# Kernel tuning notes

Measured on AMD Instinct MI355X. Metric: run time of the kernel, lower is better.

Reference implementation:

```python
import jax, jax.numpy as jnp
import numpy as np


def setup_inputs() -> dict:
    key = jax.random.key(0)
    B, C, H, W = 16, 96, 128, 128
    x = jax.random.normal(key, (B, C, H, W), dtype=jnp.float32)
    return {"x": x}


def reference(x):
    # CrossScan forward, in_channel_first=True, out_channel_first=True,
    # one_by_one=False, scans=0 (4-directional cross scan).
    B, C, H, W = x.shape
    y0 = x.reshape(B, C, H * W)                       # row-major scan
    y1 = jnp.swapaxes(x, 2, 3).reshape(B, C, H * W)   # column-major scan
    y2 = y0[..., ::-1]                                # reversed row-major
    y3 = y1[..., ::-1]                                # reversed column-major
    return jnp.stack([y0, y1, y2, y3], axis=1)        # [B, 4, C, H*W]
```

## Files before the change

kernel.cpp:

```cpp
#include <hip/hip_runtime.h>


#define Hh 128
#define Ww 128
#define HWp (Hh * Ww)
#define Cc 96
#define Bb 16
#define TILE 64

__global__ __launch_bounds__(1024) void cross_scan_kernel(
    const float* __restrict__ x, float* __restrict__ out) {
  __shared__ float tile[TILE][TILE + 1];

  const int tx = threadIdx.x;
  const int ty = threadIdx.y;
  const int tileId = blockIdx.x;
  const int tileRow = (tileId >> 1) * TILE;
  const int tileCol = (tileId & 1) * TILE;
  const int plane = blockIdx.y;
  const int b = plane / Cc;
  const int c = plane - b * Cc;

  const float* xp = x + (size_t)plane * HWp;
  float* out0 = out + ((size_t)(b * 4 + 0) * Cc + c) * HWp;
  float* out1 = out + ((size_t)(b * 4 + 1) * Cc + c) * HWp;
  float* out2 = out + ((size_t)(b * 4 + 2) * Cc + c) * HWp;
  float* out3 = out + ((size_t)(b * 4 + 3) * Cc + c) * HWp;

  const int row = tileRow + ty;
  const int col = tileCol + tx * 4;
  const int idx = row * Ww + col;

  const float4 v = *(const float4*)(xp + idx);

  *(float4*)(out0 + idx) = v;
  *(float4*)(out2 + (HWp - 4 - idx)) = make_float4(v.w, v.z, v.y, v.x);

  tile[ty][tx * 4 + 0] = v.x;
  tile[ty][tx * 4 + 1] = v.y;
  tile[ty][tx * 4 + 2] = v.z;
  tile[ty][tx * 4 + 3] = v.w;
  __syncthreads();

  float4 t;
  t.x = tile[tx * 4 + 0][ty];
  t.y = tile[tx * 4 + 1][ty];
  t.z = tile[tx * 4 + 2][ty];
  t.w = tile[tx * 4 + 3][ty];
  const int o = (tileCol + ty) * Hh + tileRow + tx * 4;
  *(float4*)(out1 + o) = t;
  *(float4*)(out3 + (HWp - 4 - o)) = make_float4(t.w, t.z, t.y, t.x);
}

extern "C" void kernel_launch(void* const* d_in, const int* in_sizes, int n_in,
                              void* d_out, int out_size, void* d_ws,
                              size_t ws_size, hipStream_t stream) {
  const float* x = (const float*)d_in[0];
  float* out = (float*)d_out;
  dim3 grid(4, Bb * Cc);
  dim3 block(16, 64);
  cross_scan_kernel<<<grid, block, 0, stream>>>(x, out);
}
```

Measured before the change: 463.0 us.

## Use smaller blocks with per-thread row loops and shared-memory reversed outputs

Shrinks blocks from 1024 to 256 threads, with each thread loading and storing four rows of the 64x64 tile. The reversed row-major and column-major outputs are now built by reading the shared tile in reverse order, so all four output streams are written with forward, aligned float4 stores. This aims to improve occupancy and memory-level parallelism on a bandwidth-bound copy. In exchange it adds extra shared-memory reads and possible bank conflicts for the reversed reads.

```diff
diff --git a/kernel.cpp b/kernel.cpp
--- a/kernel.cpp
+++ b/kernel.cpp
@@ -8,15 +8,15 @@
 #define Bb 16
 #define TILE 64
 
-__global__ __launch_bounds__(1024) void cross_scan_kernel(
+__global__ __launch_bounds__(256) void cross_scan_kernel(
     const float* __restrict__ x, float* __restrict__ out) {
   __shared__ float tile[TILE][TILE + 1];
 
   const int tx = threadIdx.x;
   const int ty = threadIdx.y;
   const int tileId = blockIdx.x;
-  const int tileRow = (tileId >> 1) * TILE;
-  const int tileCol = (tileId & 1) * TILE;
+  const int r0 = (tileId >> 1) * TILE;
+  const int c0 = (tileId & 1) * TILE;
   const int plane = blockIdx.y;
   const int b = plane / Cc;
   const int c = plane - b * Cc;
@@ -27,29 +27,54 @@
   float* out2 = out + ((size_t)(b * 4 + 2) * Cc + c) * HWp;
   float* out3 = out + ((size_t)(b * 4 + 3) * Cc + c) * HWp;
 
-  const int row = tileRow + ty;
-  const int col = tileCol + tx * 4;
-  const int idx = row * Ww + col;
-
-  const float4 v = *(const float4*)(xp + idx);
-
-  *(float4*)(out0 + idx) = v;
-  *(float4*)(out2 + (HWp - 4 - idx)) = make_float4(v.w, v.z, v.y, v.x);
-
-  tile[ty][tx * 4 + 0] = v.x;
-  tile[ty][tx * 4 + 1] = v.y;
-  tile[ty][tx * 4 + 2] = v.z;
-  tile[ty][tx * 4 + 3] = v.w;
+  float4 v[4];
+#pragma unroll
+  for (int j = 0; j < 4; ++j) {
+    const int r = ty + 16 * j;
+    v[j] = *(const float4*)(xp + (r0 + r) * Ww + c0 + tx * 4);
+  }
+#pragma unroll
+  for (int j = 0; j < 4; ++j) {
+    const int r = ty + 16 * j;
+    *(float4*)(out0 + (r0 + r) * Ww + c0 + tx * 4) = v[j];
+    tile[r][tx * 4 + 0] = v[j].x;
+    tile[r][tx * 4 + 1] = v[j].y;
+    tile[r][tx * 4 + 2] = v[j].z;
+    tile[r][tx * 4 + 3] = v[j].w;
+  }
   __syncthreads();
 
-  float4 t;
-  t.x = tile[tx * 4 + 0][ty];
-  t.y = tile[tx * 4 + 1][ty];
-  t.z = tile[tx * 4 + 2][ty];
-  t.w = tile[tx * 4 + 3][ty];
-  const int o = (tileCol + ty) * Hh + tileRow + tx * 4;
-  *(float4*)(out1 + o) = t;
-  *(float4*)(out3 + (HWp - 4 - o)) = make_float4(t.w, t.z, t.y, t.x);
+  const int r2b = TILE - r0;
+  const int c2b = TILE - c0;
+  const int R3b = TILE - c0;
+  const int c3b = TILE - r0;
+
+#pragma unroll
+  for (int j = 0; j < 4; ++j) {
+    const int R = ty + 16 * j;
+
+    float4 t1;
+    t1.x = tile[tx * 4 + 0][R];
+    t1.y = tile[tx * 4 + 1][R];
+    t1.z = tile[tx * 4 + 2][R];
+    t1.w = tile[tx * 4 + 3][R];
+    *(float4*)(out1 + (c0 + R) * Hh + r0 + tx * 4) = t1;
+
+    const float* Trow = &tile[63 - R][0];
+    float4 t2;
+    t2.x = Trow[63 - tx * 4];
+    t2.y = Trow[62 - tx * 4];
+    t2.z = Trow[61 - tx * 4];
+    t2.w = Trow[60 - tx * 4];
+    *(float4*)(out2 + (r2b + R) * Ww + c2b + tx * 4) = t2;
+
+    float4 t3;
+    t3.x = tile[63 - tx * 4][63 - R];
+    t3.y = tile[62 - tx * 4][63 - R];
+    t3.z = tile[61 - tx * 4][63 - R];
+    t3.w = tile[60 - tx * 4][63 - R];
+    *(float4*)(out3 + (R3b + R) * Hh + c3b + tx * 4) = t3;
+  }
 }
 
 extern "C" void kernel_launch(void* const* d_in, const int* in_sizes, int n_in,
@@ -58,6 +83,6 @@
   const float* x = (const float*)d_in[0];
   float* out = (float*)d_out;
   dim3 grid(4, Bb * Cc);
-  dim3 block(16, 64);
+  dim3 block(16, 16);
   cross_scan_kernel<<<grid, block, 0, stream>>>(x, out);
 }
```

Result: no change. 461.8 us (-0.2%).
